# Performance work log

Measured on AMD Instinct MI355X. Metric: run time of the kernel, lower is better.

The kernel has to match this reference:

```python
import jax, jax.numpy as jnp
import numpy as np

B, T, D, V, U = 16, 1000, 512, 5000, 64


def _safe_logaddexp(a, b):
    # logaddexp with nan-safe gradients when both args are -inf
    both = jnp.isneginf(a) & jnp.isneginf(b)
    a_ = jnp.where(both, 0.0, a)
    b_ = jnp.where(both, 0.0, b)
    return jnp.where(both, -jnp.inf, jnp.logaddexp(a_, b_))


def _log_sub_exp(a, b):
    # faithful port of log_substraction_exp: log(exp(a) - exp(b)), stable
    mask1 = (~jnp.isinf(a)) & (~jnp.isinf(b))
    a_ = jnp.where(mask1, a, -1.0)
    b_ = jnp.where(mask1, b, -2.0)
    ans_tmp = b_ + jnp.log(jnp.exp(a_ - b_) - 1.0)
    a_ = jnp.where(jnp.isinf(ans_tmp), -2000.0, a_)
    b_ = jnp.where(jnp.isinf(ans_tmp), -2001.0, b_)
    ans1 = b_ + jnp.log(jnp.exp(a_ - b_) - 1.0)
    ans = jnp.where(mask1, ans1, -jnp.inf)
    mask2 = (~jnp.isinf(a)) & jnp.isinf(b)
    return jnp.where(mask2, a, ans)


def _ctc_trellis(logp, ys):
    # Standard CTC lattice over extended labels (blank interleaved), S = 2U+1.
    # alpha[t,b,s]: logprob of paths over frames 0..t ending in state s (incl. emission at t)
    # beta[t,b,s]:  logprob of emitting frames t+1..T-1 and finishing, given state s at t
    # This reproduces the k2 lattice forward/backward scores at the label states.
    Bb, Tt, _ = logp.shape
    Uu = ys.shape[1]
    S = 2 * Uu + 1
    l_ext = jnp.zeros((Bb, S), ys.dtype).at[:, 1::2].set(ys)  # blank=0 at even s
    lp = jnp.take_along_axis(logp, jnp.broadcast_to(l_ext[:, None, :], (Bb, Tt, S)), axis=2)
    skip_ok = jnp.zeros((Bb, S), bool).at[:, 3::2].set(ys[:, 1:] != ys[:, :-1])
    lpT = jnp.transpose(lp, (1, 0, 2))  # [T,B,S]
    ninf1 = jnp.full((Bb, 1), -jnp.inf)
    ninf2 = jnp.full((Bb, 2), -jnp.inf)

    a0 = jnp.full((Bb, S), -jnp.inf).at[:, :2].set(lpT[0, :, :2])

    def astep(ap, lp_t):
        s1 = jnp.concatenate([ninf1, ap[:, :-1]], 1)
        s2 = jnp.concatenate([ninf2, ap[:, :-2]], 1)
        a = lp_t + _safe_logaddexp(_safe_logaddexp(ap, s1), jnp.where(skip_ok, s2, -jnp.inf))
        return a, a

    _, arest = jax.lax.scan(astep, a0, lpT[1:])
    alpha = jnp.concatenate([a0[None], arest], 0)  # [T,B,S]

    bl = jnp.full((Bb, S), -jnp.inf).at[:, S - 2:].set(0.0)  # final states: last label / last blank
    skipL2 = jnp.concatenate([skip_ok[:, 2:], jnp.zeros((Bb, 2), bool)], 1)

    def bstep(bn, lp_next):
        m = lp_next + bn
        m1 = jnp.concatenate([m[:, 1:], ninf1], 1)
        m2 = jnp.concatenate([m[:, 2:], ninf2], 1)
        bcur = _safe_logaddexp(_safe_logaddexp(m, m1), jnp.where(skipL2, m2, -jnp.inf))
        return bcur, bcur

    _, brest = jax.lax.scan(bstep, bl, lpT[1:], reverse=True)
    beta = jnp.concatenate([brest, bl[None]], 0)  # [T,B,S]
    return alpha, beta, lp


def setup_inputs() -> dict:
    key = jax.random.key(0)
    k1, k2, k3 = jax.random.split(key, 3)
    hs_pad = jax.random.normal(k1, (B, T, D), jnp.float32)
    hlens = jnp.full((B,), T, jnp.int32)
    ys_pad = jax.random.randint(k2, (B, U), 1, V)  # labels in [1, V); 0 is blank
    ali = jnp.zeros((B, U), jnp.int32)  # unused when risk_factor == 0
    W = jax.random.normal(k3, (D, V), jnp.float32) * 0.02
    b = jnp.zeros((V,), jnp.float32)
    return {"hs_pad": hs_pad, "hlens": hlens, "ys_pad": ys_pad, "ali": ali, "W": W, "b": b}


def reference(hs_pad, hlens, ys_pad, ali, W, b):
    # ctc_lo + log_softmax (dropout_rate=0). hlens are all equal -> sort/unsort is identity.
    logp = jax.nn.log_softmax(hs_pad @ W + b, axis=-1)  # [B,T,V]
    alpha_f, beta_f, lp = _ctc_trellis(logp, ys_pad)
    alpha = jnp.transpose(alpha_f[:, :, 1::2], (1, 2, 0))  # [B,U,T]
    beta = jnp.transpose(beta_f[:, :, 1::2], (1, 2, 0))    # [B,U,T]
    p = jnp.transpose(lp[:, :, 1::2], (0, 2, 1))           # [B,U,T] logprob of label u at frame t
    # beta', excluding re-emission of label u at t+1 -> paths whose label-u segment ends at t
    bp = _log_sub_exp(beta[:, :, :-1], beta[:, :, 1:] + p[:, :, 1:])
    bp = jnp.concatenate([bp, beta[:, :, -1:]], -1)
    loss_state = alpha + bp
    loss_state = jnp.where(jnp.isnan(loss_state), -jnp.inf, loss_state)
    loss_u = jax.nn.logsumexp(loss_state, axis=2)  # aggregate == 'time'
    mask = jnp.isinf(loss_u)
    denom = (~mask).astype(loss_u.dtype).sum(1)
    loss_fsas = jnp.where(mask, 0.0, loss_u).sum(1) / denom
    Uu = ys_pad.shape[1]
    loss_fsas = jnp.where(hlens < Uu, 0.0, loss_fsas)
    return (-loss_fsas).mean()
```

## Files before the change

### kernel.cpp

```cpp
#include <hip/hip_runtime.h>

#define NB 16
#define NT 1000
#define ND 512
#define NV 5000
#define NVP 5120
#define NU 64
#define NM (NB * NT)
#define NCH 40

typedef short short8v __attribute__((ext_vector_type(8)));
typedef float float4v __attribute__((ext_vector_type(4)));

#define NEGINF (-__builtin_inff())
#define SENTL  (-1.0e30f)
#define LOG2E 1.4426950408889634f
#define LN2F  0.6931471805599453f
#define SENT2 (-2000.4586751f * LOG2E)

__device__ __forceinline__ float fexp2(float x) { return __builtin_amdgcn_exp2f(x); }
__device__ __forceinline__ float flog2(float x) { return __builtin_amdgcn_logf(x); }

__device__ __forceinline__ float dpp_shr1(float x) {
  int xi = __builtin_bit_cast(int, x);
  int r = __builtin_amdgcn_update_dpp(xi, xi, 0x138, 0xf, 0xf, false);
  return __builtin_bit_cast(float, r);
}
__device__ __forceinline__ float dpp_shl1(float x) {
  int xi = __builtin_bit_cast(int, x);
  int r = __builtin_amdgcn_update_dpp(xi, xi, 0x130, 0xf, 0xf, false);
  return __builtin_bit_cast(float, r);
}

__device__ __forceinline__ short f2bf(float x) {
  unsigned int u = __builtin_bit_cast(unsigned int, x);
  unsigned int r = (u + 0x7fffu + ((u >> 16) & 1u)) >> 16;
  return (short)(unsigned short)r;
}
__device__ __forceinline__ float bf2f(short h) {
  unsigned int u = ((unsigned int)(unsigned short)h) << 16;
  return __builtin_bit_cast(float, u);
}

__device__ __forceinline__ void g2lds16(const short* g, short* l) {
  __builtin_amdgcn_global_load_lds(
      (const __attribute__((address_space(1))) void*)g,
      (__attribute__((address_space(3))) void*)l, 16, 0, 0);
}

__device__ __forceinline__ float lae2s(float a, float b) {
  float m = fmaxf(a, b);
  return m + flog2(fexp2(a - m) + fexp2(b - m));
}
__device__ __forceinline__ float lae3s(float a, float b, float c) {
  float m = fmaxf(fmaxf(a, b), c);
  return m + flog2(fexp2(a - m) + fexp2(b - m) + fexp2(c - m));
}
__device__ __forceinline__ float lsub2(float a, float b) {
  float tmp = b + flog2(fexp2(a - b) - 1.0f);
  if (__builtin_isinf(tmp)) tmp = SENT2;
  return tmp;
}

__global__ void k_zero(float* out) {
  if (threadIdx.x == 0) out[0] = 0.0f;
}

__global__ __launch_bounds__(256) void k_cvt_hs(const float* __restrict__ in,
                                                short* __restrict__ out) {
  size_t i = (size_t)blockIdx.x * 256 + threadIdx.x;
  const float4* p = (const float4*)in + i * 2;
  float4 v0 = p[0], v1 = p[1];
  short8v r;
  r[0] = f2bf(v0.x); r[1] = f2bf(v0.y); r[2] = f2bf(v0.z); r[3] = f2bf(v0.w);
  r[4] = f2bf(v1.x); r[5] = f2bf(v1.y); r[6] = f2bf(v1.z); r[7] = f2bf(v1.w);
  int row = (int)(i >> 6);
  int g = (int)(i & 63);
  int gs = (g & ~7) | ((g & 7) ^ (row & 7));
  *(short8v*)(out + (size_t)row * ND + gs * 8) = r;
}

__global__ __launch_bounds__(256) void k_cvt_wt(const float* __restrict__ W,
                                                short* __restrict__ WT) {
  __shared__ short tile[64 * 72];
  int n0 = blockIdx.x * 64, k0 = blockIdx.y * 64;
  int tid = threadIdx.x;
  int kr = tid >> 2, part = tid & 3;
  const float* src = W + (size_t)(k0 + kr) * NV + n0 + part * 16;
#pragma unroll
  for (int jj = 0; jj < 4; ++jj) {
    int c = n0 + part * 16 + jj * 4;
    float4 v;
    if (c + 3 < NV) {
      v = *(const float4*)(src + jj * 4);
    } else {
      v.x = (c + 0 < NV) ? src[jj * 4 + 0] : 0.f;
      v.y = (c + 1 < NV) ? src[jj * 4 + 1] : 0.f;
      v.z = (c + 2 < NV) ? src[jj * 4 + 2] : 0.f;
      v.w = (c + 3 < NV) ? src[jj * 4 + 3] : 0.f;
    }
    int base = kr * 72 + part * 16 + jj * 4;
    tile[base + 0] = f2bf(v.x); tile[base + 1] = f2bf(v.y);
    tile[base + 2] = f2bf(v.z); tile[base + 3] = f2bf(v.w);
  }
  __syncthreads();
  int n = tid & 63, kq = tid >> 6;
  int nn = n0 + n;
  if (nn < NVP) {
#pragma unroll
    for (int half = 0; half < 2; ++half) {
      short8v val;
#pragma unroll
      for (int jj = 0; jj < 8; ++jj) val[jj] = tile[(kq * 16 + half * 8 + jj) * 72 + n];
      int g = (k0 >> 3) + kq * 2 + half;
      int gs = (g & ~7) | ((g & 7) ^ (nn & 7));
      *(short8v*)(WT + (size_t)nn * ND + gs * 8) = val;
    }
  }
}

__global__ __launch_bounds__(64) void k_gather2(const float* __restrict__ W,
                                                const int* __restrict__ ys,
                                                short* __restrict__ Wg_hi,
                                                short* __restrict__ Wg_lo) {
  int u = blockIdx.x, b = blockIdx.y, t = threadIdx.x;
  short8v hi = {0,0,0,0,0,0,0,0}, lo = {0,0,0,0,0,0,0,0};
  if (u < NU + 1) {
    int lab = (u == 0) ? 0 : ys[b * NU + u - 1];
#pragma unroll
    for (int i = 0; i < 8; ++i) {
      float w = W[(size_t)(t * 8 + i) * NV + lab];
      short h = f2bf(w);
      hi[i] = h;
      lo[i] = f2bf(w - bf2f(h));
    }
  }
  int gs = (t & ~7) | ((t & 7) ^ (u & 7));
  size_t base = ((size_t)(b * 128 + u)) * ND + gs * 8;
  *(short8v*)(Wg_hi + base) = hi;
  *(short8v*)(Wg_lo + base) = lo;
}

__global__ __launch_bounds__(256) void k_labg(const short* __restrict__ hsb,
                                              const short* __restrict__ Wg_hi,
                                              const short* __restrict__ Wg_lo,
                                              const int* __restrict__ ys,
                                              const float* __restrict__ bias,
                                              float* __restrict__ ll) {
  __shared__ short As[128 * 64];
  __shared__ short Bh[128 * 64];
  __shared__ short Bl[128 * 64];

  int mt = blockIdx.x, b = blockIdx.y;
  int t0 = mt * 128;
  int tid = threadIdx.x;
  int lane = tid & 63, wave = tid >> 6;
  int wm = wave >> 1, wn = wave & 1;
  int lrow = lane & 15, lkhi = lane >> 4;

  const short* gaBase = hsb + (size_t)(b * NT + t0 + wave * 32 + (lane >> 3)) * ND + (lane & 7) * 8;
  const short* ghBase = Wg_hi + (size_t)(b * 128 + wave * 32 + (lane >> 3)) * ND + (lane & 7) * 8;
  const short* glBase = Wg_lo + (size_t)(b * 128 + wave * 32 + (lane >> 3)) * ND + (lane & 7) * 8;

  float4v acc[4][4];
#pragma unroll
  for (int m = 0; m < 4; ++m)
#pragma unroll
    for (int n = 0; n < 4; ++n)
#pragma unroll
      for (int j = 0; j < 4; ++j) acc[m][n][j] = 0.f;

  for (int s = 0; s < 8; ++s) {
    int k0 = s * 64;
#pragma unroll
    for (int i = 0; i < 4; ++i) {
      g2lds16(gaBase + (size_t)(i * 8) * ND + k0, &As[(wave * 32 + i * 8) * 64]);
      g2lds16(ghBase + (size_t)(i * 8) * ND + k0, &Bh[(wave * 32 + i * 8) * 64]);
      g2lds16(glBase + (size_t)(i * 8) * ND + k0, &Bl[(wave * 32 + i * 8) * 64]);
    }
    __syncthreads();
#pragma unroll
    for (int kk = 0; kk < 2; ++kk) {
      short8v av[4], bhv[4], blv2[4];
#pragma unroll
      for (int m = 0; m < 4; ++m) {
        int r = wm * 64 + m * 16 + lrow;
        int col = (kk * 32 + lkhi * 8) ^ ((r & 7) << 3);
        av[m] = *(const short8v*)&As[r * 64 + col];
      }
#pragma unroll
      for (int n = 0; n < 4; ++n) {
        int r = wn * 64 + n * 16 + lrow;
        int col = (kk * 32 + lkhi * 8) ^ ((r & 7) << 3);
        bhv[n] = *(const short8v*)&Bh[r * 64 + col];
        blv2[n] = *(const short8v*)&Bl[r * 64 + col];
      }
#pragma unroll
      for (int m = 0; m < 4; ++m)
#pragma unroll
        for (int n = 0; n < 4; ++n) {
          acc[m][n] = __builtin_amdgcn_mfma_f32_16x16x32_bf16(av[m], bhv[n], acc[m][n], 0, 0, 0);
          acc[m][n] = __builtin_amdgcn_mfma_f32_16x16x32_bf16(av[m], blv2[n], acc[m][n], 0, 0, 0);
        }
    }
    __syncthreads();
  }

  float bu[4]; bool uval[4];
#pragma unroll
  for (int n = 0; n < 4; ++n) {
    int u = wn * 64 + n * 16 + lrow;
    uval[n] = u < NU + 1;
    int lab = (u == 0) ? 0 : (uval[n] ? ys[b * NU + u - 1] : 0);
    bu[n] = uval[n] ? bias[lab] : 0.f;
  }
#pragma unroll
  for (int m = 0; m < 4; ++m)
#pragma unroll
    for (int j = 0; j < 4; ++j) {
      int trow = t0 + wm * 64 + m * 16 + lkhi * 4 + j;
      if (trow < NT) {
#pragma unroll
        for (int n = 0; n < 4; ++n) {
          int u = wn * 64 + n * 16 + lrow;
          if (uval[n])
            ll[((size_t)(b * 128 + u)) * NT + trow] = acc[m][n][j] + bu[n];
        }
      }
    }
}

__global__ __launch_bounds__(256) void k_denom(const short* __restrict__ hsb,
                                               const short* __restrict__ WT,
                                               const float* __restrict__ bias,
                                               float* __restrict__ pm,
                                               float* __restrict__ ps) {
  __shared__ short As[128 * 64];
  __shared__ short Ws[128 * 64];
  __shared__ float mred[128][2];
  __shared__ float sred[128][2];

  int lin = blockIdx.x;
  int wg = (lin & 7) * 625 + (lin >> 3);
  int mt = wg / NCH, chunk = wg % NCH;
  int t0 = mt * 128;
  int n0 = chunk * 128;
  int tid = threadIdx.x;
  int lane = tid & 63, wave = tid >> 6;
  int wm = wave >> 1, wn = wave & 1;
  int lrow = lane & 15, lkhi = lane >> 4;

  const short* gaBase = hsb + (size_t)(t0 + wave * 32 + (lane >> 3)) * ND + (lane & 7) * 8;
  const short* gwBase = WT + (size_t)(n0 + wave * 32 + (lane >> 3)) * ND + (lane & 7) * 8;

  float4v acc[4][4];
#pragma unroll
  for (int m = 0; m < 4; ++m)
#pragma unroll
    for (int n = 0; n < 4; ++n)
#pragma unroll
      for (int j = 0; j < 4; ++j) acc[m][n][j] = 0.f;

  auto stage = [&](int s) {
    int k0 = s * 64;
#pragma unroll
    for (int i = 0; i < 4; ++i) {
      g2lds16(gaBase + (size_t)(i * 8) * ND + k0, &As[(wave * 32 + i * 8) * 64]);
      g2lds16(gwBase + (size_t)(i * 8) * ND + k0, &Ws[(wave * 32 + i * 8) * 64]);
    }
  };
  auto compute = [&]() {
#pragma unroll
    for (int kk = 0; kk < 2; ++kk) {
      short8v av[4], wv[4];
#pragma unroll
      for (int m = 0; m < 4; ++m) {
        int r = wm * 64 + m * 16 + lrow;
        int col = (kk * 32 + lkhi * 8) ^ ((r & 7) << 3);
        av[m] = *(const short8v*)&As[r * 64 + col];
      }
#pragma unroll
      for (int n = 0; n < 4; ++n) {
        int r = wn * 64 + n * 16 + lrow;
        int col = (kk * 32 + lkhi * 8) ^ ((r & 7) << 3);
        wv[n] = *(const short8v*)&Ws[r * 64 + col];
      }
#pragma unroll
      for (int m = 0; m < 4; ++m)
#pragma unroll
        for (int n = 0; n < 4; ++n)
          acc[m][n] = __builtin_amdgcn_mfma_f32_16x16x32_bf16(av[m], wv[n], acc[m][n], 0, 0, 0);
    }
  };

  for (int s = 0; s < 8; ++s) {
    stage(s);
    __syncthreads();
    compute();
    __syncthreads();
  }

  float bcol[4]; bool cval[4];
#pragma unroll
  for (int n = 0; n < 4; ++n) {
    int c = n0 + wn * 64 + n * 16 + lrow;
    cval[n] = c < NV;
    bcol[n] = cval[n] ? bias[c] : 0.f;
  }
#pragma unroll
  for (int m = 0; m < 4; ++m)
#pragma unroll
    for (int j = 0; j < 4; ++j) {
      float mx = NEGINF;
#pragma unroll
      for (int n = 0; n < 4; ++n) {
        float v = cval[n] ? acc[m][n][j] + bcol[n] : NEGINF;
        mx = fmaxf(mx, v);
      }
#pragma unroll
      for (int d = 1; d < 16; d <<= 1) mx = fmaxf(mx, __shfl_xor(mx, d));
      float mxc = fmaxf(mx, -3.0e38f);
      float p = 0.f;
#pragma unroll
      for (int n = 0; n < 4; ++n) {
        float v = cval[n] ? acc[m][n][j] + bcol[n] : NEGINF;
        p += __expf(v - mxc);
      }
#pragma unroll
      for (int d = 1; d < 16; d <<= 1) p += __shfl_xor(p, d);
      if (lrow == 0) {
        int rloc = wm * 64 + m * 16 + lkhi * 4 + j;
        mred[rloc][wn] = mx;
        sred[rloc][wn] = p;
      }
    }
  __syncthreads();
  if (tid < 128) {
    int row = t0 + tid;
    float m0 = mred[tid][0], m1 = mred[tid][1];
    float m = fmaxf(m0, m1);
    float ss = 0.f;
    if (m != NEGINF)
      ss = ((m0 == NEGINF) ? 0.f : sred[tid][0] * __expf(m0 - m))
         + ((m1 == NEGINF) ? 0.f : sred[tid][1] * __expf(m1 - m));
    pm[(size_t)chunk * NM + row] = m;
    ps[(size_t)chunk * NM + row] = ss;
  }
}

__global__ __launch_bounds__(256) void k_dred(const float* __restrict__ pm,
                                              const float* __restrict__ ps,
                                              float* __restrict__ denom) {
  int row = blockIdx.x * 256 + threadIdx.x;
  if (row >= NM) return;
  float m = NEGINF, s = 0.f;
  for (int c = 0; c < NCH; ++c) {
    float mc = pm[(size_t)c * NM + row];
    float sc = ps[(size_t)c * NM + row];
    if (mc == NEGINF) continue;
    if (mc > m) { s = s * __expf(m - mc) + sc; m = mc; }
    else        { s += sc * __expf(mc - m); }
  }
  denom[row] = m + __logf(s);
}

__global__ __launch_bounds__(64) void k_fwdbwd(const float* __restrict__ ll,
                                               const float* __restrict__ denom,
                                               const int* __restrict__ ys,
                                               float* __restrict__ aod,
                                               float* __restrict__ bp) {
  __shared__ float denS[NT];
  __shared__ float blkS[NT];
  int bid = blockIdx.x;
  int l = threadIdx.x;
  int b = (bid < NB) ? bid : bid - NB;
  const float* llb = ll + (size_t)b * 128 * NT;
  const float* denb = denom + b * NT;
#pragma unroll
  for (int i = 0; i < 16; ++i) {
    int idx = i * 64 + l;
    if (idx < NT) { denS[idx] = denb[idx]; blkS[idx] = llb[idx]; }
  }
  __syncthreads();
  const float* lrow = llb + (size_t)(1 + l) * NT;

  if (bid < NB) {
    int lab = ys[b * NU + l];
    int labp = ys[b * NU + ((l >= 1) ? (l - 1) : 0)];
    bool skip = (l >= 1) && (lab != labp);
    float* aodb = aod + (size_t)b * NT * NU;

    float den = denS[0];
    float ae = (l == 0) ? (blkS[0] - den) * LOG2E : SENTL;
    float ao = (l == 0) ? (lrow[0] - den) * LOG2E : SENTL;
    aodb[l] = ao;

    float cl[16];
#pragma unroll
    for (int j = 0; j < 16; ++j) {
      int tt = 1 + j; if (tt > NT - 1) tt = NT - 1;
      cl[j] = lrow[tt];
    }
    for (int g = 0; g < 63; ++g) {
      float nl[16];
      if (g < 62) {
#pragma unroll
        for (int j = 0; j < 16; ++j) {
          int tt = 17 + g * 16 + j; if (tt > NT - 1) tt = NT - 1;
          nl[j] = lrow[tt];
        }
      } else {
#pragma unroll
        for (int j = 0; j < 16; ++j) nl[j] = 0.f;
      }
#pragma unroll
      for (int j = 0; j < 16; ++j) {
        int t = 1 + g * 16 + j;
        if (t < NT) {
          float d2 = denS[t];
          float pb = (blkS[t] - d2) * LOG2E, pl = (cl[j] - d2) * LOG2E;
          float po = dpp_shr1(ao); if (l == 0) po = SENTL;
          float aen = pb + lae2s(ae, po);
          float aon = pl + lae3s(ao, ae, skip ? po : SENTL);
          ae = aen; ao = aon;
          aodb[t * NU + l] = ao;
        }
      }
#pragma unroll
      for (int j = 0; j < 16; ++j) cl[j] = nl[j];
    }
  } else {
    int lab = ys[b * NU + l];
    int labn = ys[b * NU + ((l < NU - 1) ? (l + 1) : l)];
    bool skipn = (l < NU - 1) && (labn != lab);
    float* bpb = bp + (size_t)b * NT * NU;

    float bo = (l == NU - 1) ? 0.0f : SENTL;
    float be = SENTL;
    float b128 = 0.0f;
    bpb[(NT - 1) * NU + l] = bo;

    float blv[16];
#pragma unroll
    for (int j = 0; j < 16; ++j) {
      int tt = NT - 2 - j; if (tt < 0) tt = 0;
      blv[j] = lrow[tt + 1];
    }
    for (int g = 0; g < 63; ++g) {
      float nl2[16];
      if (g < 62) {
#pragma unroll
        for (int j = 0; j < 16; ++j) {
          int tt = NT - 2 - 16 * (g + 1) - j; if (tt < 0) tt = 0;
          nl2[j] = lrow[tt + 1];
        }
      } else {
#pragma unroll
        for (int j = 0; j < 16; ++j) nl2[j] = 0.f;
      }
#pragma unroll
      for (int j = 0; j < 16; ++j) {
        int t = NT - 2 - 16 * g - j;
        if (t >= 0) {
          float d2 = denS[t + 1];
          float pbv = (blkS[t + 1] - d2) * LOG2E, plv = (blv[j] - d2) * LOG2E;
          float me = pbv + be;
          float mo = plv + bo;
          float m128 = pbv + b128;
          float ne = dpp_shl1(me); if (l == NU - 1) ne = m128;
          float no = dpp_shl1(mo); if (l == NU - 1) no = SENTL;
          float ben = lae2s(me, mo);
          float bon = lae3s(mo, ne, skipn ? no : SENTL);
          bpb[t * NU + l] = lsub2(bon, mo);
          be = ben; bo = bon; b128 = m128;
        }
      }
#pragma unroll
      for (int j = 0; j < 16; ++j) blv[j] = nl2[j];
    }
  }
}

__global__ __launch_bounds__(512) void k_loss(const float* __restrict__ aod,
                                              const float* __restrict__ bp,
                                              const int* __restrict__ hlens,
                                              float* __restrict__ out) {
  __shared__ float ms[8][64], ss[8][64];
  int b = blockIdx.x, tid = threadIdx.x;
  int w = tid >> 6, l = tid & 63;
  const float* ab = aod + (size_t)b * NT * NU;
  const float* pb = bp + (size_t)b * NT * NU;
  float m = NEGINF, s = 0.f;
  int t0 = w * 125, t1 = t0 + 125;
  for (int t = t0; t < t1; ++t) {
    float x = ab[t * NU + l] + pb[t * NU + l];
    if (__builtin_isnan(x) || x < -1.0e29f) continue;
    if (x > m) { s = s * fexp2(m - x) + 1.0f; m = x; }
    else       { s += fexp2(x - m); }
  }
  ms[w][l] = m; ss[w][l] = s;
  __syncthreads();
  if (w == 0) {
    float mm = NEGINF;
#pragma unroll
    for (int i = 0; i < 8; ++i) mm = fmaxf(mm, ms[i][l]);
    float lu;
    if (mm == NEGINF) lu = NEGINF;
    else {
      float st = 0.f;
#pragma unroll
      for (int i = 0; i < 8; ++i)
        st += (ms[i][l] == NEGINF) ? 0.f : ss[i][l] * fexp2(ms[i][l] - mm);
      lu = (mm + flog2(st)) * LN2F;
    }
    bool msk = __builtin_isinf(lu);
    float sv = msk ? 0.f : lu;
    float cv = msk ? 0.f : 1.f;
#pragma unroll
    for (int d = 1; d < 64; d <<= 1) { sv += __shfl_xor(sv, d); cv += __shfl_xor(cv, d); }
    if (l == 0) {
      float lf = sv / cv;
      if (hlens[b] < NU) lf = 0.f;
      atomicAdd(out, -lf * (1.0f / NB));
    }
  }
}

extern "C" void kernel_launch(void* const* d_in, const int* in_sizes, int n_in,
                              void* d_out, int out_size, void* d_ws, size_t ws_size,
                              hipStream_t stream) {
  const float* hs    = (const float*)d_in[0];
  const int*   hlens = (const int*)d_in[1];
  const int*   ys    = (const int*)d_in[2];
  const float* W     = (const float*)d_in[4];
  const float* bias  = (const float*)d_in[5];
  float* out = (float*)d_out;

  char* ws = (char*)d_ws;
  short* hsb   = (short*)(ws + 0);
  short* WT    = (short*)(ws + 16384000);
  float* pm    = (float*)(ws + 21626880);
  float* psv   = (float*)(ws + 24186880);
  float* dnm   = (float*)(ws + 26746880);
  float* ll    = (float*)(ws + 26810880);
  short* Wg_hi = (short*)(ws + 16384000);
  short* Wg_lo = (short*)(ws + 18481152);
  float* aod   = (float*)(ws + 0);
  float* bpb   = (float*)(ws + 4096000);

  k_zero<<<1, 64, 0, stream>>>(out);
  k_cvt_hs<<<4000, 256, 0, stream>>>(hs, hsb);
  k_cvt_wt<<<dim3(80, 8), 256, 0, stream>>>(W, WT);
  k_denom<<<5000, 256, 0, stream>>>(hsb, WT, bias, pm, psv);
  k_dred<<<63, 256, 0, stream>>>(pm, psv, dnm);
  k_gather2<<<dim3(128, 16), 64, 0, stream>>>(W, ys, Wg_hi, Wg_lo);
  k_labg<<<dim3(8, 16), 256, 0, stream>>>(hsb, Wg_hi, Wg_lo, ys, bias, ll);
  k_fwdbwd<<<32, 64, 0, stream>>>(ll, dnm, ys, aod, bpb);
  k_loss<<<16, 512, 0, stream>>>(aod, bpb, hlens, out);
}
```

Measured before the change: 374.1 us.

## Precompute bf16 hi/lo weight split in transpose, gather rows, remap denom tiles

The weight conversion kernel now also writes a bf16 residual (lo) copy of the transposed weights. The label gather then reads contiguous swizzled rows of both copies instead of doing strided column reads from the fp32 W. The denom GEMM block-to-tile mapping is regrouped so that 8 M-tiles share each weight chunk, which is meant to improve L2 reuse. The label-logit buffer stride shrinks to 72 rows per batch, and workspace offsets are rearranged. The cost is extra write traffic and more LDS in the transpose kernel.

```diff
diff --git a/kernel.cpp b/kernel.cpp
--- a/kernel.cpp
+++ b/kernel.cpp
@@ -6,6 +6,7 @@
 #define NV 5000
 #define NVP 5120
 #define NU 64
+#define NLL 72
 #define NM (NB * NT)
 #define NCH 40
 
@@ -81,8 +82,10 @@
 }
 
 __global__ __launch_bounds__(256) void k_cvt_wt(const float* __restrict__ W,
-                                                short* __restrict__ WT) {
-  __shared__ short tile[64 * 72];
+                                                short* __restrict__ WT,
+                                                short* __restrict__ WTlo) {
+  __shared__ short tileH[64 * 72];
+  __shared__ short tileL[64 * 72];
   int n0 = blockIdx.x * 64, k0 = blockIdx.y * 64;
   int tid = threadIdx.x;
   int kr = tid >> 2, part = tid & 3;
@@ -100,8 +103,13 @@
       v.w = (c + 3 < NV) ? src[jj * 4 + 3] : 0.f;
     }
     int base = kr * 72 + part * 16 + jj * 4;
-    tile[base + 0] = f2bf(v.x); tile[base + 1] = f2bf(v.y);
-    tile[base + 2] = f2bf(v.z); tile[base + 3] = f2bf(v.w);
+    float vv[4] = {v.x, v.y, v.z, v.w};
+#pragma unroll
+    for (int q = 0; q < 4; ++q) {
+      short h = f2bf(vv[q]);
+      tileH[base + q] = h;
+      tileL[base + q] = f2bf(vv[q] - bf2f(h));
+    }
   }
   __syncthreads();
   int n = tid & 63, kq = tid >> 6;
@@ -109,17 +117,22 @@
   if (nn < NVP) {
 #pragma unroll
     for (int half = 0; half < 2; ++half) {
-      short8v val;
-#pragma unroll
-      for (int jj = 0; jj < 8; ++jj) val[jj] = tile[(kq * 16 + half * 8 + jj) * 72 + n];
+      short8v vh, vl;
+#pragma unroll
+      for (int jj = 0; jj < 8; ++jj) {
+        vh[jj] = tileH[(kq * 16 + half * 8 + jj) * 72 + n];
+        vl[jj] = tileL[(kq * 16 + half * 8 + jj) * 72 + n];
+      }
       int g = (k0 >> 3) + kq * 2 + half;
       int gs = (g & ~7) | ((g & 7) ^ (nn & 7));
-      *(short8v*)(WT + (size_t)nn * ND + gs * 8) = val;
-    }
-  }
-}
-
-__global__ __launch_bounds__(64) void k_gather2(const float* __restrict__ W,
+      *(short8v*)(WT + (size_t)nn * ND + gs * 8) = vh;
+      *(short8v*)(WTlo + (size_t)nn * ND + gs * 8) = vl;
+    }
+  }
+}
+
+__global__ __launch_bounds__(64) void k_gather2(const short* __restrict__ WT,
+                                                const short* __restrict__ WTlo,
                                                 const int* __restrict__ ys,
                                                 short* __restrict__ Wg_hi,
                                                 short* __restrict__ Wg_lo) {
@@ -127,16 +140,12 @@
   short8v hi = {0,0,0,0,0,0,0,0}, lo = {0,0,0,0,0,0,0,0};
   if (u < NU + 1) {
     int lab = (u == 0) ? 0 : ys[b * NU + u - 1];
-#pragma unroll
-    for (int i = 0; i < 8; ++i) {
-      float w = W[(size_t)(t * 8 + i) * NV + lab];
-      short h = f2bf(w);
-      hi[i] = h;
-      lo[i] = f2bf(w - bf2f(h));
-    }
-  }
-  int gs = (t & ~7) | ((t & 7) ^ (u & 7));
-  size_t base = ((size_t)(b * 128 + u)) * ND + gs * 8;
+    int ps = (t & ~7) | ((t & 7) ^ (lab & 7));
+    hi = *(const short8v*)(WT + (size_t)lab * ND + ps * 8);
+    lo = *(const short8v*)(WTlo + (size_t)lab * ND + ps * 8);
+  }
+  int q = (t & ~7) | ((t & 7) ^ (u & 7));
+  size_t base = ((size_t)(b * 128 + u)) * ND + q * 8;
   *(short8v*)(Wg_hi + base) = hi;
   *(short8v*)(Wg_lo + base) = lo;
 }
@@ -224,7 +233,7 @@
         for (int n = 0; n < 4; ++n) {
           int u = wn * 64 + n * 16 + lrow;
           if (uval[n])
-            ll[((size_t)(b * 128 + u)) * NT + trow] = acc[m][n][j] + bu[n];
+            ll[((size_t)(b * NLL + u)) * NT + trow] = acc[m][n][j] + bu[n];
         }
       }
     }
@@ -241,8 +250,17 @@
   __shared__ float sred[128][2];
 
   int lin = blockIdx.x;
-  int wg = (lin & 7) * 625 + (lin >> 3);
-  int mt = wg / NCH, chunk = wg % NCH;
+  int o = (lin & 7) * 625 + (lin >> 3);
+  int mt, chunk;
+  if (o < 4800) {
+    int sb = o / 320, w = o % 320;
+    mt = sb * 8 + (w & 7);
+    chunk = w >> 3;
+  } else {
+    int w = o - 4800;
+    mt = 120 + (w % 5);
+    chunk = w / 5;
+  }
   int t0 = mt * 128;
   int n0 = chunk * 128;
   int tid = threadIdx.x;
@@ -374,7 +392,7 @@
   int bid = blockIdx.x;
   int l = threadIdx.x;
   int b = (bid < NB) ? bid : bid - NB;
-  const float* llb = ll + (size_t)b * 128 * NT;
+  const float* llb = ll + (size_t)b * NLL * NT;
   const float* denb = denom + b * NT;
 #pragma unroll
   for (int i = 0; i < 16; ++i) {
@@ -539,21 +557,22 @@
   char* ws = (char*)d_ws;
   short* hsb   = (short*)(ws + 0);
   short* WT    = (short*)(ws + 16384000);
-  float* pm    = (float*)(ws + 21626880);
-  float* psv   = (float*)(ws + 24186880);
-  float* dnm   = (float*)(ws + 26746880);
-  float* ll    = (float*)(ws + 26810880);
-  short* Wg_hi = (short*)(ws + 16384000);
-  short* Wg_lo = (short*)(ws + 18481152);
+  short* WTlo  = (short*)(ws + 21626880);
+  float* pm    = (float*)(ws + 26869760);
+  float* psv   = (float*)(ws + 29429760);
+  float* dnm   = (float*)(ws + 31989760);
+  float* ll    = (float*)(ws + 32053760);
+  short* Wg_hi = (short*)(ws + 26869760);
+  short* Wg_lo = (short*)(ws + 28966912);
   float* aod   = (float*)(ws + 0);
   float* bpb   = (float*)(ws + 4096000);
 
   k_zero<<<1, 64, 0, stream>>>(out);
   k_cvt_hs<<<4000, 256, 0, stream>>>(hs, hsb);
-  k_cvt_wt<<<dim3(80, 8), 256, 0, stream>>>(W, WT);
+  k_cvt_wt<<<dim3(80, 8), 256, 0, stream>>>(W, WT, WTlo);
   k_denom<<<5000, 256, 0, stream>>>(hsb, WT, bias, pm, psv);
   k_dred<<<63, 256, 0, stream>>>(pm, psv, dnm);
-  k_gather2<<<dim3(128, 16), 64, 0, stream>>>(W, ys, Wg_hi, Wg_lo);
+  k_gather2<<<dim3(128, 16), 64, 0, stream>>>(WT, WTlo, ys, Wg_hi, Wg_lo);
   k_labg<<<dim3(8, 16), 256, 0, stream>>>(hsb, Wg_hi, Wg_lo, ys, bias, ll);
   k_fwdbwd<<<32, 64, 0, stream>>>(ll, dnm, ys, aod, bpb);
   k_loss<<<16, 512, 0, stream>>>(aod, bpb, hlens, out);
```

After: 365.6 us. 1.02x faster.
